# Kernel tuning notes

Hardware: AMD Instinct MI355X
Metric: run time of the kernel (lower is better)

Reference implementation:

```python
import jax, jax.numpy as jnp
import numpy as np

HIDDEN = 2048
INTER = 1408
N_EXPERTS = 16
TOP_K = 2


def setup_inputs() -> dict:
    key = jax.random.key(0)
    ks = jax.random.split(key, 5)
    hidden_states = jax.random.normal(ks[0], (4, 2048, HIDDEN), dtype=jnp.float32)
    gate_w = jax.random.normal(ks[1], (N_EXPERTS, HIDDEN), dtype=jnp.float32) * 0.02  # router Linear(D,E) weight
    wg = jax.random.normal(ks[2], (N_EXPERTS, HIDDEN, INTER), dtype=jnp.float32) * 0.02  # gate_proj
    wu = jax.random.normal(ks[3], (N_EXPERTS, HIDDEN, INTER), dtype=jnp.float32) * 0.02  # up_proj
    wd = jax.random.normal(ks[4], (N_EXPERTS, INTER, HIDDEN), dtype=jnp.float32) * 0.02  # down_proj
    return {"hidden_states": hidden_states, "gate_w": gate_w, "wg": wg, "wu": wu, "wd": wd}


def reference(hidden_states, gate_w, wg, wu, wd):
    B, T, D = hidden_states.shape
    E = gate_w.shape[0]
    x = hidden_states.reshape(-1, D)  # [N, D]
    N = x.shape[0]

    # Router: softmax in fp32, then top-k
    logits = x @ gate_w.T  # [N, E]
    probs = jax.nn.softmax(logits.astype(jnp.float32), axis=-1)
    rw, sel = jax.lax.top_k(probs, TOP_K)  # [N, K]
    rw = rw / jnp.sum(rw, axis=-1, keepdims=True)  # norm_topk_prob=True
    rw = rw.astype(x.dtype)

    # Scatter top-k weights into dense per-expert combine weights [N, E]
    cw = jnp.zeros((N, E), dtype=x.dtype).at[jnp.arange(N)[:, None], sel].add(rw)

    # Accumulate weighted SwiGLU expert outputs; scan keeps memory at O(N*I)
    def body(acc, ws):
        wg_e, wu_e, wd_e, w_e = ws  # [D,I], [D,I], [I,D], [N]
        h = jax.nn.silu(x @ wg_e) * (x @ wu_e)  # [N, I]
        return acc + w_e[:, None] * (h @ wd_e), None

    out, _ = jax.lax.scan(body, jnp.zeros_like(x), (wg, wu, wd, cw.T))
    return out.reshape(B, T, D)
```

## Files before the change

### kernel.cpp

```cpp
#include <hip/hip_runtime.h>

#define D 2048
#define I_DIM 1408
#define E_NUM 16
#define NTOK 8192
#define BK 32
#define BK2 64

typedef _Float16 half8 __attribute__((ext_vector_type(8)));
typedef float float4v __attribute__((ext_vector_type(4)));

#define GLL16(gp, lp)                                                        \
    __builtin_amdgcn_global_load_lds(                                        \
        (const __attribute__((address_space(1))) void*)(gp),                 \
        (__attribute__((address_space(3))) void*)(lp), 16, 0, 0)


__global__ __launch_bounds__(256) void router_kernel(
    const float* __restrict__ x, const float* __restrict__ gw,
    _Float16* __restrict__ xb, int* __restrict__ counts,
    int* __restrict__ ids, float* __restrict__ wts, float* __restrict__ wtk)
{
    int t = blockIdx.x * 4 + (threadIdx.x >> 6);
    int lane = threadIdx.x & 63;
    const float* xr = x + (size_t)t * D;

    float acc[E_NUM];
#pragma unroll
    for (int e = 0; e < E_NUM; ++e) acc[e] = 0.f;

#pragma unroll 4
    for (int i = 0; i < D / 64; ++i) {
        int d = lane + i * 64;
        float xv = xr[d];
        xb[(size_t)t * D + d] = (_Float16)xv;
#pragma unroll
        for (int e = 0; e < E_NUM; ++e)
            acc[e] = fmaf(xv, gw[e * D + d], acc[e]);
    }
#pragma unroll
    for (int e = 0; e < E_NUM; ++e) {
        float v = acc[e];
#pragma unroll
        for (int m = 32; m >= 1; m >>= 1) v += __shfl_xor(v, m, 64);
        acc[e] = v;
    }
    if (lane == 0) {
        int e1 = 0; float l1 = acc[0];
#pragma unroll
        for (int e = 1; e < E_NUM; ++e)
            if (acc[e] > l1) { l1 = acc[e]; e1 = e; }
        int e2 = -1; float l2 = -3.0e38f;
#pragma unroll
        for (int e = 0; e < E_NUM; ++e) {
            if (e == e1) continue;
            if (acc[e] > l2) { l2 = acc[e]; e2 = e; }
        }
        float w1 = 1.f / (1.f + expf(l2 - l1));
        float w2 = 1.f - w1;
        int s1 = atomicAdd(&counts[e1], 1);
        ids[e1 * NTOK + s1] = t * 2;     wts[e1 * NTOK + s1] = w1;
        int s2 = atomicAdd(&counts[e2], 1);
        ids[e2 * NTOK + s2] = t * 2 + 1; wts[e2 * NTOK + s2] = w2;
        wtk[t * 2] = w1; wtk[t * 2 + 1] = w2;
    }
}

__global__ __launch_bounds__(256) void transpose_cvt_kernel(
    const float* __restrict__ src, _Float16* __restrict__ dst, int K, int N)
{
    int e = blockIdx.z;
    int k0 = blockIdx.x * 64;
    int n0 = blockIdx.y * 64;
    const float* s = src + (size_t)e * K * N + (size_t)k0 * N + n0;
    _Float16* d = dst + (size_t)e * N * K + (size_t)n0 * K + k0;

    __shared__ float T[64][65];
    int tid = threadIdx.x;
    int kl = tid >> 4;
    int n4 = (tid & 15) * 4;
#pragma unroll
    for (int p = 0; p < 4; ++p) {
        int k = p * 16 + kl;
        float4 v = *(const float4*)(s + (size_t)k * N + n4);
        T[n4 + 0][k] = v.x;
        T[n4 + 1][k] = v.y;
        T[n4 + 2][k] = v.z;
        T[n4 + 3][k] = v.w;
    }
    __syncthreads();
    int nl = tid >> 3;
    int kc = (tid & 7) * 8;
#pragma unroll
    for (int q = 0; q < 2; ++q) {
        int n = q * 32 + nl;
        half8 v;
#pragma unroll
        for (int j = 0; j < 8; ++j) v[j] = (_Float16)T[n][kc + j];
        *(half8*)(d + (size_t)n * K + kc) = v;
    }
}

__global__ __launch_bounds__(256, 2) void moe_gateup_f16(
    const _Float16* __restrict__ xb,
    const _Float16* __restrict__ wgt, const _Float16* __restrict__ wut,
    const int* __restrict__ counts, const int* __restrict__ ids,
    _Float16* __restrict__ h)
{
    int b = blockIdx.x;
    int g = b % 176;
    int m0 = (b / 176) * 128;
    int e = g / 11;
    int n0 = (g % 11) * 128;
    int cnt = counts[e];
    if (m0 >= cnt) return;

    __shared__ __align__(16) _Float16 Als[128 * BK2];
    __shared__ __align__(16) _Float16 Bg[128 * BK2];
    __shared__ __align__(16) _Float16 Bu[128 * BK2];
    __shared__ int rid[128];

    int tid = threadIdx.x;
    if (tid < 128) {
        int slot = m0 + tid;
        rid[tid] = (slot < cnt) ? ids[e * NTOK + slot] : -1;
    }
    __syncthreads();

    const _Float16* wgE = wgt + (size_t)e * I_DIM * D;
    const _Float16* wuE = wut + (size_t)e * I_DIM * D;

    int wave = tid >> 6, lane = tid & 63;
    int wm = (wave & 1) * 64, wn = (wave >> 1) * 64;
    int lc = lane & 15, lq = lane >> 4;
    int lr8 = lane >> 3;
    int gseg = ((lane & 7) ^ lr8) * 8;

    float4v accG[4][4], accU[4][4];
#pragma unroll
    for (int a = 0; a < 4; ++a)
#pragma unroll
        for (int c = 0; c < 4; ++c) {
            accG[a][c] = (float4v){0.f, 0.f, 0.f, 0.f};
            accU[a][c] = (float4v){0.f, 0.f, 0.f, 0.f};
        }

    for (int k0 = 0; k0 < D; k0 += BK2) {
#pragma unroll
        for (int c = 0; c < 4; ++c) {
            int r0 = wave * 32 + c * 8;
            int row = r0 + lr8;
            int id = rid[row];
            int tr = (id >= 0) ? (id >> 1) : 0;
            GLL16(xb + (size_t)tr * D + k0 + gseg, &Als[r0 * BK2]);
            GLL16(wgE + (size_t)(n0 + row) * D + k0 + gseg, &Bg[r0 * BK2]);
            GLL16(wuE + (size_t)(n0 + row) * D + k0 + gseg, &Bu[r0 * BK2]);
        }
        __syncthreads();

#pragma unroll
        for (int ks = 0; ks < 2; ++ks) {
            half8 af[4];
#pragma unroll
            for (int ms = 0; ms < 4; ++ms) {
                int row = wm + ms * 16 + lc;
                int s = (ks * 4 + lq) ^ (row & 7);
                af[ms] = *(const half8*)(&Als[row * BK2 + s * 8]);
            }
#pragma unroll
            for (int ns = 0; ns < 4; ++ns) {
                int row = wn + ns * 16 + lc;
                int s = (ks * 4 + lq) ^ (row & 7);
                half8 bg = *(const half8*)(&Bg[row * BK2 + s * 8]);
                half8 bu = *(const half8*)(&Bu[row * BK2 + s * 8]);
#pragma unroll
                for (int ms = 0; ms < 4; ++ms) {
                    accG[ms][ns] = __builtin_amdgcn_mfma_f32_16x16x32_f16(af[ms], bg, accG[ms][ns], 0, 0, 0);
                    accU[ms][ns] = __builtin_amdgcn_mfma_f32_16x16x32_f16(af[ms], bu, accU[ms][ns], 0, 0, 0);
                }
            }
        }
        __syncthreads();
    }

#pragma unroll
    for (int ms = 0; ms < 4; ++ms) {
#pragma unroll
        for (int r = 0; r < 4; ++r) {
            int row = wm + ms * 16 + lq * 4 + r;
            int id = rid[row];
            if (id >= 0) {
                _Float16* hr = h + (size_t)id * I_DIM + n0;
#pragma unroll
                for (int ns = 0; ns < 4; ++ns) {
                    float gv = accG[ms][ns][r];
                    float uv = accU[ms][ns][r];
                    float sv = gv / (1.f + expf(-gv)) * uv;
                    hr[wn + ns * 16 + lc] = (_Float16)sv;
                }
            }
        }
    }
}

__global__ __launch_bounds__(256, 2) void moe_down_f16(
    const _Float16* __restrict__ h, const _Float16* __restrict__ wdt,
    const int* __restrict__ counts, const int* __restrict__ ids,
    _Float16* __restrict__ part)
{
    int b = blockIdx.x;
    int g = b % 256;
    int m0 = (b / 256) * 128;
    int e = g >> 4;
    int n0 = (g & 15) * 128;
    int cnt = counts[e];
    if (m0 >= cnt) return;

    __shared__ __align__(16) _Float16 Als[128 * BK2];
    __shared__ __align__(16) _Float16 Bd[128 * BK2];
    __shared__ int rid[128];

    int tid = threadIdx.x;
    if (tid < 128) {
        int slot = m0 + tid;
        rid[tid] = (slot < cnt) ? ids[e * NTOK + slot] : -1;
    }
    __syncthreads();

    const _Float16* wdE = wdt + (size_t)e * D * I_DIM;

    int wave = tid >> 6, lane = tid & 63;
    int wm = (wave & 1) * 64, wn = (wave >> 1) * 64;
    int lc = lane & 15, lq = lane >> 4;
    int lr8 = lane >> 3;
    int gseg = ((lane & 7) ^ lr8) * 8;

    float4v acc[4][4];
#pragma unroll
    for (int a = 0; a < 4; ++a)
#pragma unroll
        for (int c = 0; c < 4; ++c)
            acc[a][c] = (float4v){0.f, 0.f, 0.f, 0.f};

    for (int k0 = 0; k0 < I_DIM; k0 += BK2) {
#pragma unroll
        for (int c = 0; c < 4; ++c) {
            int r0 = wave * 32 + c * 8;
            int row = r0 + lr8;
            int id = rid[row];
            int tr = (id >= 0) ? id : 0;
            GLL16(h + (size_t)tr * I_DIM + k0 + gseg, &Als[r0 * BK2]);
            GLL16(wdE + (size_t)(n0 + row) * I_DIM + k0 + gseg, &Bd[r0 * BK2]);
        }
        __syncthreads();

#pragma unroll
        for (int ks = 0; ks < 2; ++ks) {
            half8 af[4];
#pragma unroll
            for (int ms = 0; ms < 4; ++ms) {
                int row = wm + ms * 16 + lc;
                int s = (ks * 4 + lq) ^ (row & 7);
                af[ms] = *(const half8*)(&Als[row * BK2 + s * 8]);
            }
#pragma unroll
            for (int ns = 0; ns < 4; ++ns) {
                int row = wn + ns * 16 + lc;
                int s = (ks * 4 + lq) ^ (row & 7);
                half8 bd = *(const half8*)(&Bd[row * BK2 + s * 8]);
#pragma unroll
                for (int ms = 0; ms < 4; ++ms)
                    acc[ms][ns] = __builtin_amdgcn_mfma_f32_16x16x32_f16(af[ms], bd, acc[ms][ns], 0, 0, 0);
            }
        }
        __syncthreads();
    }

#pragma unroll
    for (int ms = 0; ms < 4; ++ms) {
#pragma unroll
        for (int r = 0; r < 4; ++r) {
            int row = wm + ms * 16 + lq * 4 + r;
            int id = rid[row];
            if (id >= 0) {
                _Float16* pr = part + (size_t)id * D + n0;
#pragma unroll
                for (int ns = 0; ns < 4; ++ns)
                    pr[wn + ns * 16 + lc] = (_Float16)acc[ms][ns][r];
            }
        }
    }
}

__global__ __launch_bounds__(256) void combine_kernel(
    const _Float16* __restrict__ part, const float* __restrict__ wtk,
    float* __restrict__ out)
{
    int t = blockIdx.x;
    int tid = threadIdx.x;
    float w1 = wtk[2 * t], w2 = wtk[2 * t + 1];
    const _Float16* p1 = part + (size_t)(2 * t) * D;
    const _Float16* p2 = p1 + D;
    float* o = out + (size_t)t * D;
    int i = tid * 8;
    half8 a = *(const half8*)(p1 + i);
    half8 bvec = *(const half8*)(p2 + i);
#pragma unroll
    for (int j = 0; j < 8; ++j)
        o[i + j] = w1 * (float)a[j] + w2 * (float)bvec[j];
}

__global__ __launch_bounds__(256, 2) void moe_gateup_old(
    const _Float16* __restrict__ xb,
    const float* __restrict__ wg, const float* __restrict__ wu,
    const int* __restrict__ counts, const int* __restrict__ ids,
    _Float16* __restrict__ h)
{
    int e = blockIdx.z;
    int cnt = counts[e];
    int m0 = blockIdx.x * 128;
    if (m0 >= cnt) return;
    int n0 = blockIdx.y * 128;

    __shared__ __align__(16) _Float16 Als[128 * BK];
    __shared__ __align__(16) _Float16 Bg[BK * 128];
    __shared__ __align__(16) _Float16 Bu[BK * 128];
    __shared__ int rid[128];

    int tid = threadIdx.x;
    if (tid < 128) {
        int slot = m0 + tid;
        rid[tid] = (slot < cnt) ? ids[e * NTOK + slot] : -1;
    }
    __syncthreads();

    const float* wgE = wg + (size_t)e * D * I_DIM;
    const float* wuE = wu + (size_t)e * D * I_DIM;

    int wave = tid >> 6, lane = tid & 63;
    int wm = (wave & 1) * 64, wn = (wave >> 1) * 64;
    int lc = lane & 15, lq = lane >> 4;

    float4v accG[4][4], accU[4][4];
#pragma unroll
    for (int a = 0; a < 4; ++a)
#pragma unroll
        for (int c = 0; c < 4; ++c) {
            accG[a][c] = (float4v){0.f, 0.f, 0.f, 0.f};
            accU[a][c] = (float4v){0.f, 0.f, 0.f, 0.f};
        }

    int nn = tid & 127;
    int kb2 = tid >> 7;

    for (int k0 = 0; k0 < D; k0 += BK) {
#pragma unroll
        for (int cc = 0; cc < 2; ++cc) {
            int c = tid + cc * 256;
            int row = c >> 2, kc = c & 3;
            int id = rid[row];
            uint4 v = {0u, 0u, 0u, 0u};
            if (id >= 0)
                v = *(const uint4*)(xb + (size_t)(id >> 1) * D + k0 + kc * 8);
            *(uint4*)(&Als[row * BK + kc * 8]) = v;
        }
#pragma unroll
        for (int kk = 0; kk < 2; ++kk) {
            int kb = kb2 * 2 + kk;
            const float* pg = wgE + (size_t)(k0 + kb * 8) * I_DIM + n0 + nn;
            const float* pu = wuE + (size_t)(k0 + kb * 8) * I_DIM + n0 + nn;
            half8 hg, hu;
#pragma unroll
            for (int j = 0; j < 8; ++j) {
                hg[j] = (_Float16)pg[(size_t)j * I_DIM];
                hu[j] = (_Float16)pu[(size_t)j * I_DIM];
            }
            *(half8*)(&Bg[(kb * 128 + nn) * 8]) = hg;
            *(half8*)(&Bu[(kb * 128 + nn) * 8]) = hu;
        }
        __syncthreads();

        half8 af[4];
#pragma unroll
        for (int ms = 0; ms < 4; ++ms)
            af[ms] = *(const half8*)(&Als[(wm + ms * 16 + lc) * BK + lq * 8]);
#pragma unroll
        for (int ns = 0; ns < 4; ++ns) {
            half8 bg = *(const half8*)(&Bg[(lq * 128 + wn + ns * 16 + lc) * 8]);
            half8 bu = *(const half8*)(&Bu[(lq * 128 + wn + ns * 16 + lc) * 8]);
#pragma unroll
            for (int ms = 0; ms < 4; ++ms) {
                accG[ms][ns] = __builtin_amdgcn_mfma_f32_16x16x32_f16(af[ms], bg, accG[ms][ns], 0, 0, 0);
                accU[ms][ns] = __builtin_amdgcn_mfma_f32_16x16x32_f16(af[ms], bu, accU[ms][ns], 0, 0, 0);
            }
        }
        __syncthreads();
    }

#pragma unroll
    for (int ms = 0; ms < 4; ++ms) {
#pragma unroll
        for (int r = 0; r < 4; ++r) {
            int row = wm + ms * 16 + lq * 4 + r;
            int id = rid[row];
            if (id >= 0) {
                _Float16* hr = h + (size_t)id * I_DIM + n0;
#pragma unroll
                for (int ns = 0; ns < 4; ++ns) {
                    float gv = accG[ms][ns][r];
                    float uv = accU[ms][ns][r];
                    float sv = gv / (1.f + expf(-gv)) * uv;
                    hr[wn + ns * 16 + lc] = (_Float16)sv;
                }
            }
        }
    }
}

__global__ __launch_bounds__(256, 2) void moe_down_old(
    const _Float16* __restrict__ h, const float* __restrict__ wd,
    const int* __restrict__ counts, const int* __restrict__ ids,
    const float* __restrict__ wts, float* __restrict__ out)
{
    int e = blockIdx.z;
    int cnt = counts[e];
    int m0 = blockIdx.x * 128;
    if (m0 >= cnt) return;
    int n0 = blockIdx.y * 128;

    __shared__ __align__(16) _Float16 Als[128 * BK];
    __shared__ __align__(16) _Float16 Bd[BK * 128];
    __shared__ int rid[128];
    __shared__ float rw[128];

    int tid = threadIdx.x;
    if (tid < 128) {
        int slot = m0 + tid;
        int ok = slot < cnt;
        rid[tid] = ok ? ids[e * NTOK + slot] : -1;
        rw[tid]  = ok ? wts[e * NTOK + slot] : 0.f;
    }
    __syncthreads();

    const float* wdE = wd + (size_t)e * I_DIM * D;

    int wave = tid >> 6, lane = tid & 63;
    int wm = (wave & 1) * 64, wn = (wave >> 1) * 64;
    int lc = lane & 15, lq = lane >> 4;

    float4v acc[4][4];
#pragma unroll
    for (int a = 0; a < 4; ++a)
#pragma unroll
        for (int c = 0; c < 4; ++c)
            acc[a][c] = (float4v){0.f, 0.f, 0.f, 0.f};

    int nn = tid & 127;
    int kb2 = tid >> 7;

    for (int k0 = 0; k0 < I_DIM; k0 += BK) {
#pragma unroll
        for (int cc = 0; cc < 2; ++cc) {
            int c = tid + cc * 256;
            int row = c >> 2, kc = c & 3;
            int id = rid[row];
            uint4 v = {0u, 0u, 0u, 0u};
            if (id >= 0)
                v = *(const uint4*)(h + (size_t)id * I_DIM + k0 + kc * 8);
            *(uint4*)(&Als[row * BK + kc * 8]) = v;
        }
#pragma unroll
        for (int kk = 0; kk < 2; ++kk) {
            int kb = kb2 * 2 + kk;
            const float* pd = wdE + (size_t)(k0 + kb * 8) * D + n0 + nn;
            half8 hd;
#pragma unroll
            for (int j = 0; j < 8; ++j)
                hd[j] = (_Float16)pd[(size_t)j * D];
            *(half8*)(&Bd[(kb * 128 + nn) * 8]) = hd;
        }
        __syncthreads();

        half8 af[4];
#pragma unroll
        for (int ms = 0; ms < 4; ++ms)
            af[ms] = *(const half8*)(&Als[(wm + ms * 16 + lc) * BK + lq * 8]);
#pragma unroll
        for (int ns = 0; ns < 4; ++ns) {
            half8 bd = *(const half8*)(&Bd[(lq * 128 + wn + ns * 16 + lc) * 8]);
#pragma unroll
            for (int ms = 0; ms < 4; ++ms)
                acc[ms][ns] = __builtin_amdgcn_mfma_f32_16x16x32_f16(af[ms], bd, acc[ms][ns], 0, 0, 0);
        }
        __syncthreads();
    }

#pragma unroll
    for (int ms = 0; ms < 4; ++ms) {
#pragma unroll
        for (int r = 0; r < 4; ++r) {
            int row = wm + ms * 16 + lq * 4 + r;
            int id = rid[row];
            if (id >= 0) {
                int tok = id >> 1;
                float w = rw[row];
                float* orow = out + (size_t)tok * D + n0;
#pragma unroll
                for (int ns = 0; ns < 4; ++ns)
                    atomicAdd(&orow[wn + ns * 16 + lc], acc[ms][ns][r] * w);
            }
        }
    }
}

extern "C" void kernel_launch(void* const* d_in, const int* in_sizes, int n_in,
                              void* d_out, int out_size, void* d_ws, size_t ws_size,
                              hipStream_t stream) {
    const float* x  = (const float*)d_in[0];
    const float* gw = (const float*)d_in[1];
    const float* wg = (const float*)d_in[2];
    const float* wu = (const float*)d_in[3];
    const float* wd = (const float*)d_in[4];
    float* out = (float*)d_out;

    char* ws = (char*)d_ws;
    const size_t FAST_NEED = 265356288ull;

    if (ws_size >= FAST_NEED) {
        int*      counts = (int*)(ws);
        int*      ids    = (int*)(ws + 1024);
        float*    wts    = (float*)(ws + 525312);
        float*    wtk    = (float*)(ws + 1049600);
        _Float16* xb     = (_Float16*)(ws + 1115136);
        _Float16* hbuf   = (_Float16*)(ws + 34669568);
        _Float16* wgt    = (_Float16*)(ws + 80806912);
        _Float16* wut    = (_Float16*)(ws + 173081600);
        _Float16* wdt    = wgt;
        _Float16* part   = wut;

        hipMemsetAsync(counts, 0, 1024, stream);
        router_kernel<<<dim3(NTOK / 4), dim3(256), 0, stream>>>(x, gw, xb, counts, ids, wts, wtk);
        transpose_cvt_kernel<<<dim3(D / 64, I_DIM / 64, E_NUM), dim3(256), 0, stream>>>(wg, wgt, D, I_DIM);
        transpose_cvt_kernel<<<dim3(D / 64, I_DIM / 64, E_NUM), dim3(256), 0, stream>>>(wu, wut, D, I_DIM);
        moe_gateup_f16<<<dim3(176 * 64), dim3(256), 0, stream>>>(xb, wgt, wut, counts, ids, hbuf);
        transpose_cvt_kernel<<<dim3(I_DIM / 64, D / 64, E_NUM), dim3(256), 0, stream>>>(wd, wdt, I_DIM, D);
        moe_down_f16<<<dim3(256 * 64), dim3(256), 0, stream>>>(hbuf, wdt, counts, ids, part);
        combine_kernel<<<dim3(NTOK), dim3(256), 0, stream>>>(part, wtk, out);
    } else {
        int*      counts = (int*)(ws);
        int*      ids    = (int*)(ws + 1024);
        float*    wts    = (float*)(ws + 525312);
        _Float16* xb     = (_Float16*)(ws + 1049600);
        _Float16* hbuf   = (_Float16*)(ws + 34604032);
        float*    wtk    = (float*)(ws + 80741376);

        hipMemsetAsync(counts, 0, 1024, stream);
        hipMemsetAsync(d_out, 0, (size_t)out_size * sizeof(float), stream);
        router_kernel<<<dim3(NTOK / 4), dim3(256), 0, stream>>>(x, gw, xb, counts, ids, wts, wtk);
        moe_gateup_old<<<dim3(64, I_DIM / 128, E_NUM), dim3(256), 0, stream>>>(xb, wg, wu, counts, ids, hbuf);
        moe_down_old<<<dim3(64, D / 128, E_NUM), dim3(256), 0, stream>>>(hbuf, wd, counts, ids, wts, out);
    }
}
```

Baseline: 1.203 ms.

## Fuse router and weight transposes into one prep kernel; double-buffer down GEMM

Merges the router and the three fp32-to-fp16 weight transpose launches into a single prep kernel dispatched by block index. When the workspace is large enough, down_proj gets its own buffer so it can be transposed up front. The down-projection GEMM now double-buffers its LDS tiles, issuing the next K-slice's global-to-LDS loads before computing on the current one. This aims to cut launch gaps and expose load/compute overlap, at the cost of twice the LDS per block in the down kernel (lower occupancy) and more workspace.

```diff
diff --git a/kernel.cpp b/kernel.cpp
--- a/kernel.cpp
+++ b/kernel.cpp
@@ -16,12 +16,11 @@
         (__attribute__((address_space(3))) void*)(lp), 16, 0, 0)
 
 
-__global__ __launch_bounds__(256) void router_kernel(
-    const float* __restrict__ x, const float* __restrict__ gw,
+__device__ __forceinline__ void router_body(
+    int t, const float* __restrict__ x, const float* __restrict__ gw,
     _Float16* __restrict__ xb, int* __restrict__ counts,
     int* __restrict__ ids, float* __restrict__ wts, float* __restrict__ wtk)
 {
-    int t = blockIdx.x * 4 + (threadIdx.x >> 6);
     int lane = threadIdx.x & 63;
     const float* xr = x + (size_t)t * D;
 
@@ -66,16 +65,12 @@
     }
 }
 
-__global__ __launch_bounds__(256) void transpose_cvt_kernel(
-    const float* __restrict__ src, _Float16* __restrict__ dst, int K, int N)
-{
-    int e = blockIdx.z;
-    int k0 = blockIdx.x * 64;
-    int n0 = blockIdx.y * 64;
+__device__ __forceinline__ void transpose_tile(
+    const float* __restrict__ src, _Float16* __restrict__ dst,
+    int K, int N, int k0, int n0, int e, float (*T)[65])
+{
     const float* s = src + (size_t)e * K * N + (size_t)k0 * N + n0;
     _Float16* d = dst + (size_t)e * N * K + (size_t)n0 * K + k0;
-
-    __shared__ float T[64][65];
     int tid = threadIdx.x;
     int kl = tid >> 4;
     int n4 = (tid & 15) * 4;
@@ -99,6 +94,47 @@
         for (int j = 0; j < 8; ++j) v[j] = (_Float16)T[n][kc + j];
         *(half8*)(d + (size_t)n * K + kc) = v;
     }
+}
+
+#define PREP_R   2048
+#define PREP_TS  11264
+__global__ __launch_bounds__(256) void prep_kernel(
+    const float* __restrict__ x, const float* __restrict__ gw,
+    _Float16* __restrict__ xb, int* __restrict__ counts,
+    int* __restrict__ ids, float* __restrict__ wts, float* __restrict__ wtk,
+    const float* __restrict__ wg, _Float16* __restrict__ wgt,
+    const float* __restrict__ wu, _Float16* __restrict__ wut,
+    const float* __restrict__ wd, _Float16* __restrict__ wdt)
+{
+    __shared__ float T[64][65];
+    int b = blockIdx.x;
+    if (b < PREP_R) {
+        router_body(b * 4 + (threadIdx.x >> 6), x, gw, xb, counts, ids, wts, wtk);
+        return;
+    }
+    b -= PREP_R;
+    if (b < PREP_TS) {
+        int bx = b % 32, by = (b / 32) % 22, e = b / 704;
+        transpose_tile(wg, wgt, D, I_DIM, bx * 64, by * 64, e, T);
+        return;
+    }
+    b -= PREP_TS;
+    if (b < PREP_TS) {
+        int bx = b % 32, by = (b / 32) % 22, e = b / 704;
+        transpose_tile(wu, wut, D, I_DIM, bx * 64, by * 64, e, T);
+        return;
+    }
+    b -= PREP_TS;
+    int bx = b % 22, by = (b / 22) % 32, e = b / 704;
+    transpose_tile(wd, wdt, I_DIM, D, bx * 64, by * 64, e, T);
+}
+
+__global__ __launch_bounds__(256) void transpose_cvt_kernel(
+    const float* __restrict__ src, _Float16* __restrict__ dst, int K, int N)
+{
+    __shared__ float T[64][65];
+    int e = blockIdx.z;
+    transpose_tile(src, dst, K, N, blockIdx.x * 64, blockIdx.y * 64, e, T);
 }
 
 __global__ __launch_bounds__(256, 2) void moe_gateup_f16(
@@ -216,8 +252,8 @@
     int cnt = counts[e];
     if (m0 >= cnt) return;
 
-    __shared__ __align__(16) _Float16 Als[128 * BK2];
-    __shared__ __align__(16) _Float16 Bd[128 * BK2];
+    __shared__ __align__(16) _Float16 Als[2][128 * BK2];
+    __shared__ __align__(16) _Float16 Bd[2][128 * BK2];
     __shared__ int rid[128];
 
     int tid = threadIdx.x;
@@ -242,17 +278,27 @@
         for (int c = 0; c < 4; ++c)
             acc[a][c] = (float4v){0.f, 0.f, 0.f, 0.f};
 
+#define DOWN_STAGE(buf, kk0)                                                  \
+    do {                                                                      \
+        _Pragma("unroll")                                                     \
+        for (int c = 0; c < 4; ++c) {                                         \
+            int r0 = wave * 32 + c * 8;                                       \
+            int row = r0 + lr8;                                               \
+            int id = rid[row];                                                \
+            int tr = (id >= 0) ? id : 0;                                      \
+            GLL16(h + (size_t)tr * I_DIM + (kk0) + gseg, &Als[buf][r0 * BK2]);\
+            GLL16(wdE + (size_t)(n0 + row) * I_DIM + (kk0) + gseg,            \
+                  &Bd[buf][r0 * BK2]);                                        \
+        }                                                                     \
+    } while (0)
+
+    DOWN_STAGE(0, 0);
+    __syncthreads();
+
+    int cur = 0;
     for (int k0 = 0; k0 < I_DIM; k0 += BK2) {
-#pragma unroll
-        for (int c = 0; c < 4; ++c) {
-            int r0 = wave * 32 + c * 8;
-            int row = r0 + lr8;
-            int id = rid[row];
-            int tr = (id >= 0) ? id : 0;
-            GLL16(h + (size_t)tr * I_DIM + k0 + gseg, &Als[r0 * BK2]);
-            GLL16(wdE + (size_t)(n0 + row) * I_DIM + k0 + gseg, &Bd[r0 * BK2]);
-        }
-        __syncthreads();
+        int nxt = k0 + BK2;
+        if (nxt < I_DIM) DOWN_STAGE(cur ^ 1, nxt);
 
 #pragma unroll
         for (int ks = 0; ks < 2; ++ks) {
@@ -261,20 +307,22 @@
             for (int ms = 0; ms < 4; ++ms) {
                 int row = wm + ms * 16 + lc;
                 int s = (ks * 4 + lq) ^ (row & 7);
-                af[ms] = *(const half8*)(&Als[row * BK2 + s * 8]);
+                af[ms] = *(const half8*)(&Als[cur][row * BK2 + s * 8]);
             }
 #pragma unroll
             for (int ns = 0; ns < 4; ++ns) {
                 int row = wn + ns * 16 + lc;
                 int s = (ks * 4 + lq) ^ (row & 7);
-                half8 bd = *(const half8*)(&Bd[row * BK2 + s * 8]);
+                half8 bd = *(const half8*)(&Bd[cur][row * BK2 + s * 8]);
 #pragma unroll
                 for (int ms = 0; ms < 4; ++ms)
                     acc[ms][ns] = __builtin_amdgcn_mfma_f32_16x16x32_f16(af[ms], bd, acc[ms][ns], 0, 0, 0);
             }
         }
         __syncthreads();
-    }
+        cur ^= 1;
+    }
+#undef DOWN_STAGE
 
 #pragma unroll
     for (int ms = 0; ms < 4; ++ms) {
@@ -310,6 +358,14 @@
         o[i + j] = w1 * (float)a[j] + w2 * (float)bvec[j];
 }
 
+__global__ __launch_bounds__(256) void router_kernel(
+    const float* __restrict__ x, const float* __restrict__ gw,
+    _Float16* __restrict__ xb, int* __restrict__ counts,
+    int* __restrict__ ids, float* __restrict__ wts, float* __restrict__ wtk)
+{
+    router_body(blockIdx.x * 4 + (threadIdx.x >> 6), x, gw, xb, counts, ids, wts, wtk);
+}
+
 __global__ __launch_bounds__(256, 2) void moe_gateup_old(
     const _Float16* __restrict__ xb,
     const float* __restrict__ wg, const float* __restrict__ wu,
@@ -524,9 +580,10 @@
     float* out = (float*)d_out;
 
     char* ws = (char*)d_ws;
-    const size_t FAST_NEED = 265356288ull;
-
-    if (ws_size >= FAST_NEED) {
+    const size_t NEED_B = 265356288ull;
+    const size_t NEED_A = 357630976ull;
+
+    if (ws_size >= NEED_B) {
         int*      counts = (int*)(ws);
         int*      ids    = (int*)(ws + 1024);
         float*    wts    = (float*)(ws + 525312);
@@ -535,16 +592,24 @@
         _Float16* hbuf   = (_Float16*)(ws + 34669568);
         _Float16* wgt    = (_Float16*)(ws + 80806912);
         _Float16* wut    = (_Float16*)(ws + 173081600);
-        _Float16* wdt    = wgt;
         _Float16* part   = wut;
 
         hipMemsetAsync(counts, 0, 1024, stream);
-        router_kernel<<<dim3(NTOK / 4), dim3(256), 0, stream>>>(x, gw, xb, counts, ids, wts, wtk);
-        transpose_cvt_kernel<<<dim3(D / 64, I_DIM / 64, E_NUM), dim3(256), 0, stream>>>(wg, wgt, D, I_DIM);
-        transpose_cvt_kernel<<<dim3(D / 64, I_DIM / 64, E_NUM), dim3(256), 0, stream>>>(wu, wut, D, I_DIM);
-        moe_gateup_f16<<<dim3(176 * 64), dim3(256), 0, stream>>>(xb, wgt, wut, counts, ids, hbuf);
-        transpose_cvt_kernel<<<dim3(I_DIM / 64, D / 64, E_NUM), dim3(256), 0, stream>>>(wd, wdt, I_DIM, D);
-        moe_down_f16<<<dim3(256 * 64), dim3(256), 0, stream>>>(hbuf, wdt, counts, ids, part);
+
+        if (ws_size >= NEED_A) {
+            _Float16* wdt = (_Float16*)(ws + 265356288);
+            prep_kernel<<<dim3(PREP_R + 3 * PREP_TS), dim3(256), 0, stream>>>(
+                x, gw, xb, counts, ids, wts, wtk, wg, wgt, wu, wut, wd, wdt);
+            moe_gateup_f16<<<dim3(176 * 64), dim3(256), 0, stream>>>(xb, wgt, wut, counts, ids, hbuf);
+            moe_down_f16<<<dim3(256 * 64), dim3(256), 0, stream>>>(hbuf, wdt, counts, ids, part);
+        } else {
+            _Float16* wdt = wgt;
+            prep_kernel<<<dim3(PREP_R + 2 * PREP_TS), dim3(256), 0, stream>>>(
+                x, gw, xb, counts, ids, wts, wtk, wg, wgt, wu, wut, wd, wdt);
+            moe_gateup_f16<<<dim3(176 * 64), dim3(256), 0, stream>>>(xb, wgt, wut, counts, ids, hbuf);
+            transpose_cvt_kernel<<<dim3(I_DIM / 64, D / 64, E_NUM), dim3(256), 0, stream>>>(wd, wdt, I_DIM, D);
+            moe_down_f16<<<dim3(256 * 64), dim3(256), 0, stream>>>(hbuf, wdt, counts, ids, part);
+        }
         combine_kernel<<<dim3(NTOK), dim3(256), 0, stream>>>(part, wtk, out);
     } else {
         int*      counts = (int*)(ws);
```

Result: no change. 1.180 ms (-1.9%).
